# Optimization experiments

Hardware: AMD Instinct MI355X
Metric: run time of the kernel (lower is better)

The kernel has to match this reference:

```python
import jax, jax.numpy as jnp
import numpy as np

N, S, EMB, H = 4, 2048, 512, 8
D = EMB // H  # 64


def setup_inputs() -> dict:
    key = jax.random.key(0)
    ks = jax.random.split(key, 10)
    sc = 0.02
    return {
        "x": jax.random.normal(ks[0], (N, S, EMB), dtype=jnp.float32),
        "Wq": jax.random.normal(ks[1], (D, D), dtype=jnp.float32) * sc,
        "bq": jax.random.normal(ks[2], (D,), dtype=jnp.float32) * sc,
        "Wk": jax.random.normal(ks[3], (D, D), dtype=jnp.float32) * sc,
        "bk": jax.random.normal(ks[4], (D,), dtype=jnp.float32) * sc,
        "Wv": jax.random.normal(ks[5], (D, D), dtype=jnp.float32) * sc,
        "bv": jax.random.normal(ks[6], (D,), dtype=jnp.float32) * sc,
        "E": jax.random.normal(ks[7], (1, S, D), dtype=jnp.float32),
        "Wo": jax.random.normal(ks[8], (EMB, EMB), dtype=jnp.float32) * sc,
        "bo": jax.random.normal(ks[9], (EMB,), dtype=jnp.float32) * sc,
    }


def reference(x, Wq, bq, Wk, bk, Wv, bv, E, Wo, bo):
    n, s, emb = x.shape
    h, d = H, D
    xh = x.reshape(n, s, h, d)
    # per-head Linear projections (torch Linear: y = x @ W.T + b)
    q = xh @ Wq.T + bq  # [n,s,h,d]
    k = xh @ Wk.T + bk
    v = xh @ Wv.T + bv

    # QE = queries.transpose(1,2) @ E.transpose(1,2) -> [n,h,s,s]
    QE = jnp.einsum('nqhd,sd->nhqs', q, E[0])
    # _mask_positions: zero where triu(ones(S,S),1) flipped along columns == 1
    triu1 = jnp.triu(jnp.ones((s, s), dtype=bool), 1)
    QE = jnp.where(triu1[:, ::-1], 0.0, QE)
    # _skew: pad last dim on the left, reinterpret (s, s+1) as (s+1, s), drop first row
    padded = jnp.pad(QE, ((0, 0), (0, 0), (0, 0), (1, 0)))  # [n,h,s,s+1]
    Smat = padded.reshape(n, h, s + 1, s)[:, :, 1:, :]  # [n,h,s,s]

    qk = jnp.einsum('nqhd,nkhd->nhqk', q, k)
    # faithful to source: fill where mask==0 (lower triangle incl. diag) with -1e20
    qk = jnp.where(triu1, qk, jnp.float32(-1e20))
    attention = jax.nn.softmax(qk / (emb ** 0.5), axis=3) + Smat

    z = jnp.einsum('nhql,nlhd->nqhd', attention, v).reshape(n, s, h * d)
    return z @ Wo.T + bo


if __name__ == "__main__":
    out = reference(**setup_inputs())
    print(out.shape, out.dtype)
```

## Files before the change

### kernel.cpp

```cpp
#include <hip/hip_runtime.h>
#include <hip/hip_bf16.h>

#define S_LEN 2048
#define EMB   512
#define NH    8
#define DH    64
#define NB    4

typedef float f32x4  __attribute__((ext_vector_type(4)));
typedef short short8 __attribute__((ext_vector_type(8)));

__device__ __forceinline__ unsigned short f2bf_rn(float f) {
    return __builtin_bit_cast(unsigned short, __float2bfloat16(f));
}

__device__ __forceinline__ f32x4 mfma16(short8 a, short8 b, f32x4 c) {
    return __builtin_amdgcn_mfma_f32_16x16x32_bf16(a, b, c, 0, 0, 0);
}

__device__ __forceinline__ short8 frag_read(const unsigned short* lds, int row, int oct)
{
    const char* src = (const char*)lds + row * 128 + ((oct * 16) ^ ((row & 7) << 4));
    return *reinterpret_cast<const short8*>(src);
}

__device__ __forceinline__ int pinv(int k) {
    return (k & 32) + ((k >> 2) & 3) * 8 + (k & 3) + ((k & 16) >> 2);
}

__device__ __forceinline__ void stage_tile_f32(const float* __restrict__ g,
                                               int gstride, unsigned short* lds, int tid)
{
    #pragma unroll
    for (int c = tid; c < 512; c += 256) {
        const int r = c >> 3, s = c & 7;
        const float4* src = (const float4*)(g + (size_t)r * gstride + s * 8);
        const float4 a = src[0], b = src[1];
        short8 f;
        f[0] = (short)f2bf_rn(a.x); f[1] = (short)f2bf_rn(a.y);
        f[2] = (short)f2bf_rn(a.z); f[3] = (short)f2bf_rn(a.w);
        f[4] = (short)f2bf_rn(b.x); f[5] = (short)f2bf_rn(b.y);
        f[6] = (short)f2bf_rn(b.z); f[7] = (short)f2bf_rn(b.w);
        char* dst = (char*)lds + r * 128 + ((s * 16) ^ ((r & 7) << 4));
        *reinterpret_cast<short8*>(dst) = f;
    }
}

__device__ __forceinline__ void softmax_pack(const f32x4 C[4], bool diag, int w, int og,
                                             int rowg, float& dsum, short8& pa0, short8& pa1)
{
    constexpr float SM_SCALE = 0.04419417382415922f;
    float rsum = 0.f;
    unsigned short pw[16];
    if (!diag) {
        #pragma unroll
        for (int t = 0; t < 4; ++t)
            #pragma unroll
            for (int r = 0; r < 4; ++r) {
                const float wv = __expf(C[t][r] * SM_SCALE);
                rsum += wv;
                pw[t * 4 + r] = f2bf_rn(wv);
            }
    } else {
        #pragma unroll
        for (int t = 0; t < 4; ++t)
            #pragma unroll
            for (int r = 0; r < 4; ++r) {
                const bool keep = (t > w) || (t == w && (og * 4 + r) > rowg);
                const float wv = keep ? __expf(C[t][r] * SM_SCALE) : 0.f;
                rsum += wv;
                pw[t * 4 + r] = f2bf_rn(wv);
            }
    }
    dsum += rsum;
    #pragma unroll
    for (int i = 0; i < 8; ++i) { pa0[i] = (short)pw[i]; pa1[i] = (short)pw[8 + i]; }
}

__global__ __launch_bounds__(256) void qkv_mfma(
    const float* __restrict__ x,
    const float* __restrict__ Wq, const float* __restrict__ bq,
    const float* __restrict__ Wk, const float* __restrict__ bk,
    const float* __restrict__ Wv, const float* __restrict__ bv,
    unsigned short* __restrict__ qg, unsigned short* __restrict__ kg,
    unsigned short* __restrict__ vg)
{
    __shared__ unsigned short w_lds[3][64 * 64];

    const int tid  = threadIdx.x;
    const int lane = tid & 63;
    const int w    = tid >> 6;
    const int rowg = lane & 15;
    const int og   = lane >> 4;

    stage_tile_f32(Wq, 64, w_lds[0], tid);
    stage_tile_f32(Wk, 64, w_lds[1], tid);
    stage_tile_f32(Wv, 64, w_lds[2], tid);

    float bias[3][4];
    #pragma unroll
    for (int t = 0; t < 4; ++t) {
        bias[0][t] = bq[16 * t + rowg];
        bias[1][t] = bk[16 * t + rowg];
        bias[2][t] = bv[16 * t + rowg];
    }

    const int m0 = blockIdx.x * 64 + 16 * w;
    const float* xr = x + (size_t)(m0 + rowg) * 64;
    const float4 a0 = *(const float4*)(xr + og * 8);
    const float4 a1 = *(const float4*)(xr + og * 8 + 4);
    const float4 a2 = *(const float4*)(xr + 32 + og * 8);
    const float4 a3 = *(const float4*)(xr + 32 + og * 8 + 4);
    short8 af0, af1;
    af0[0] = (short)f2bf_rn(a0.x); af0[1] = (short)f2bf_rn(a0.y);
    af0[2] = (short)f2bf_rn(a0.z); af0[3] = (short)f2bf_rn(a0.w);
    af0[4] = (short)f2bf_rn(a1.x); af0[5] = (short)f2bf_rn(a1.y);
    af0[6] = (short)f2bf_rn(a1.z); af0[7] = (short)f2bf_rn(a1.w);
    af1[0] = (short)f2bf_rn(a2.x); af1[1] = (short)f2bf_rn(a2.y);
    af1[2] = (short)f2bf_rn(a2.z); af1[3] = (short)f2bf_rn(a2.w);
    af1[4] = (short)f2bf_rn(a3.x); af1[5] = (short)f2bf_rn(a3.y);
    af1[6] = (short)f2bf_rn(a3.z); af1[7] = (short)f2bf_rn(a3.w);

    __syncthreads();

    f32x4 acc[3][4];
    #pragma unroll
    for (int m = 0; m < 3; ++m)
        #pragma unroll
        for (int t = 0; t < 4; ++t) {
            const float b = bias[m][t];
            acc[m][t] = (f32x4){b, b, b, b};
        }

    #pragma unroll
    for (int m = 0; m < 3; ++m)
        #pragma unroll
        for (int t = 0; t < 4; ++t) {
            acc[m][t] = mfma16(af0, frag_read(w_lds[m], 16 * t + rowg, og),     acc[m][t]);
            acc[m][t] = mfma16(af1, frag_read(w_lds[m], 16 * t + rowg, og + 4), acc[m][t]);
        }

    unsigned short* outp[3] = {qg, kg, vg};
    #pragma unroll
    for (int m = 0; m < 3; ++m)
        #pragma unroll
        for (int r = 0; r < 4; ++r) {
            const int mr = (blockIdx.x * 64 + 16 * w) + og * 4 + r;
            const int tk = mr >> 3, h = mr & 7;
            const int n = tk >> 11, s = tk & 2047;
            const size_t rowb = (((size_t)(n * NH + h)) * S_LEN + s) * 64;
            #pragma unroll
            for (int t = 0; t < 4; ++t)
                outp[m][rowb + 16 * t + rowg] = f2bf_rn(acc[m][t][r]);
        }
}

__global__ __launch_bounds__(256) void transpose_v(
    const unsigned short* __restrict__ v, unsigned short* __restrict__ vt)
{
    __shared__ unsigned short t_lds[64][72];
    const int bid = blockIdx.x;
    const int st = bid % (S_LEN / 64);
    const int nh = bid / (S_LEN / 64);
    const unsigned short* vp = v + ((size_t)nh * S_LEN + st * 64) * DH;
    unsigned short* vtp = vt + (size_t)nh * DH * S_LEN + st * 64;
    const int tid = threadIdx.x;
    #pragma unroll
    for (int c = tid; c < 512; c += 256) {
        const int r = c >> 3, s = c & 7;
        short8 xv = *reinterpret_cast<const short8*>(vp + r * DH + s * 8);
        #pragma unroll
        for (int i = 0; i < 8; ++i) t_lds[s * 8 + i][r] = (unsigned short)xv[i];
    }
    __syncthreads();
    #pragma unroll
    for (int c = tid; c < 512; c += 256) {
        const int d = c >> 3, sc = c & 7;
        const int cb = ((sc & 4) << 3) + (sc & 3) * 4;
        short8 y;
        #pragma unroll
        for (int i = 0; i < 8; ++i)
            y[i] = (short)t_lds[d][cb + (i & 3) + ((i & 4) << 2)];
        *reinterpret_cast<short8*>(vtp + (size_t)d * S_LEN + sc * 8) = y;
    }
}

__global__ __launch_bounds__(256) void prep_e(
    const float* __restrict__ E, unsigned short* __restrict__ eb)
{
    const int i = blockIdx.x * 256 + threadIdx.x;
    if (i >= S_LEN * DH) return;
    const int dlt = i >> 6, d = i & 63;
    eb[i] = f2bf_rn(E[(size_t)(S_LEN - 1 - dlt) * DH + d]);
}

__global__ __launch_bounds__(256) void attn_mfma(
    const unsigned short* __restrict__ qg,
    const unsigned short* __restrict__ kg,
    const unsigned short* __restrict__ vtg,
    const unsigned short* __restrict__ eg,
    unsigned short* __restrict__ z)
{
    __shared__ unsigned short kbuf[2][64 * 64];
    __shared__ unsigned short vbuf[2][64 * 64];
    __shared__ unsigned short p_lds[2][64 * 64];

    constexpr float UNI = 1.0f / 2048.0f;

    const int nqt = S_LEN / 64;
    const int bid = blockIdx.x;
    const int qt  = (nqt - 1) - (bid >> 5);
    const int nh  = bid & 31;
    const int q0  = qt * 64;
    const size_t base = (size_t)nh * S_LEN * DH;
    const unsigned short* qp = qg + base;
    const unsigned short* kp = kg + base;
    const unsigned short* vp = vtg + base;

    const int tid  = threadIdx.x;
    const int lane = tid & 63;
    const int w    = tid >> 6;
    const int rowg = lane & 15;
    const int og   = lane >> 4;

    const int r0 = tid >> 3,  s0 = tid & 7;
    const int r1 = r0 + 32;
    const int ldsoff0 = r0 * 128 + ((s0 * 16) ^ ((r0 & 7) << 4));
    const int ldsoff1 = r1 * 128 + ((s0 * 16) ^ ((r1 & 7) << 4));
    const int ksrc0 = r0 * 64 + s0 * 8,    ksrc1 = r1 * 64 + s0 * 8;
    const int vsrc0 = r0 * S_LEN + s0 * 8, vsrc1 = r1 * S_LEN + s0 * 8;

    short8 kr0, kr1, vr0, vr1;

    short8 qa0, qa1;
    {
        const unsigned short* qr = qp + (size_t)(q0 + 16 * w + rowg) * DH + og * 8;
        qa0 = *reinterpret_cast<const short8*>(qr);
        qa1 = *reinterpret_cast<const short8*>(qr + 32);
    }

    const f32x4 zero4 = {0.f, 0.f, 0.f, 0.f};
    f32x4 accS[4], accR[4];
    #pragma unroll
    for (int t = 0; t < 4; ++t) { accS[t] = zero4; accR[t] = zero4; }
    float dsum = 0.f;

    kr0 = *(const short8*)(kp + (size_t)q0 * 64 + ksrc0);
    kr1 = *(const short8*)(kp + (size_t)q0 * 64 + ksrc1);
    vr0 = *(const short8*)(vp + q0 + vsrc0);
    vr1 = *(const short8*)(vp + q0 + vsrc1);
    *(short8*)((char*)kbuf[0] + ldsoff0) = kr0;
    *(short8*)((char*)kbuf[0] + ldsoff1) = kr1;
    *(short8*)((char*)vbuf[0] + ldsoff0) = vr0;
    *(short8*)((char*)vbuf[0] + ldsoff1) = vr1;
    __syncthreads();

    int cur = 0;
    for (int k0 = q0; k0 < S_LEN; k0 += 64) {
        const bool pf = (k0 + 64 < S_LEN);
        if (pf) {
            const unsigned short* kb = kp + (size_t)(k0 + 64) * 64;
            const unsigned short* vb = vp + (k0 + 64);
            kr0 = *(const short8*)(kb + ksrc0);
            kr1 = *(const short8*)(kb + ksrc1);
            vr0 = *(const short8*)(vb + vsrc0);
            vr1 = *(const short8*)(vb + vsrc1);
        }
        const unsigned short* klds = kbuf[cur];
        const unsigned short* vlds = vbuf[cur];

        f32x4 C[4];
        #pragma unroll
        for (int t = 0; t < 4; ++t) {
            const short8 kf0 = frag_read(klds, 16 * t + rowg, og);
            const short8 kf1 = frag_read(klds, 16 * t + rowg, og + 4);
            C[t] = mfma16(kf1, qa1, mfma16(kf0, qa0, zero4));
        }
        short8 pa0, pa1;
        softmax_pack(C, k0 == q0, w, og, rowg, dsum, pa0, pa1);

        #pragma unroll
        for (int tt = 0; tt < 4; ++tt) {
            const short8 vf0 = frag_read(vlds, 16 * tt + rowg, og);
            const short8 vf1 = frag_read(vlds, 16 * tt + rowg, og + 4);
            accS[tt] = mfma16(pa1, vf1, mfma16(pa0, vf0, accS[tt]));
        }

        if (pf) {
            *(short8*)((char*)kbuf[cur ^ 1] + ldsoff0) = kr0;
            *(short8*)((char*)kbuf[cur ^ 1] + ldsoff1) = kr1;
            *(short8*)((char*)vbuf[cur ^ 1] + ldsoff0) = vr0;
            *(short8*)((char*)vbuf[cur ^ 1] + ldsoff1) = vr1;
        }
        __syncthreads();
        cur ^= 1;
    }

    const int jmax = q0 >> 6;
    {
        const short8 z8 = {0, 0, 0, 0, 0, 0, 0, 0};
        #pragma unroll
        for (int c2 = 0; c2 < 2; ++c2) {
            const int cc = lane + 64 * c2;
            const int r = 16 * w + (cc >> 3), sc = cc & 7;
            *reinterpret_cast<short8*>((char*)p_lds[0] + r * 128 + sc * 16) = z8;
        }
    }
    kr0 = *(const short8*)(eg + ksrc0);
    kr1 = *(const short8*)(eg + ksrc1);
    vr0 = *(const short8*)(vp + q0 + vsrc0);
    vr1 = *(const short8*)(vp + q0 + vsrc1);
    *(short8*)((char*)kbuf[0] + ldsoff0) = kr0;
    *(short8*)((char*)kbuf[0] + ldsoff1) = kr1;
    *(short8*)((char*)vbuf[0] + ldsoff0) = vr0;
    *(short8*)((char*)vbuf[0] + ldsoff1) = vr1;
    __syncthreads();

    int cur2 = 0;
    for (int j = 0; j <= jmax; ++j) {
        const bool pf = (j < jmax);
        if (pf) {
            const unsigned short* ebn = eg + (size_t)(j + 1) * 4096;
            const unsigned short* vbn = vp + (q0 - 64 * (j + 1));
            kr0 = *(const short8*)(ebn + ksrc0);
            kr1 = *(const short8*)(ebn + ksrc1);
            vr0 = *(const short8*)(vbn + vsrc0);
            vr1 = *(const short8*)(vbn + vsrc1);
        }
        const unsigned short* elds = kbuf[cur2];
        const unsigned short* vlds = vbuf[cur2];

        f32x4 G[4];
        #pragma unroll
        for (int t = 0; t < 4; ++t)
            G[t] = mfma16(qa1, frag_read(elds, 16 * t + rowg, og + 4),
                   mfma16(qa0, frag_read(elds, 16 * t + rowg, og), zero4));

        unsigned short* pc = p_lds[j & 1];
        unsigned short* pn = p_lds[(j + 1) & 1];
        #pragma unroll
        for (int t = 0; t < 4; ++t) {
            const int c = 16 * t + rowg;
            #pragma unroll
            for (int r = 0; r < 4; ++r) {
                const int qq = 16 * w + og * 4 + r;
                float val = G[t][r];
                if (q0 + qq == S_LEN - 1) val += UNI;
                const unsigned short bv = f2bf_rn(val);
                const int swz = (qq & 7) << 4;
                if (c <= qq) {
                    const int p = pinv(qq - c);
                    *(unsigned short*)((char*)pc + qq * 128 + ((p * 2) ^ swz)) = bv;
                } else if (pf) {
                    const int p = pinv(qq - c + 64);
                    *(unsigned short*)((char*)pn + qq * 128 + ((p * 2) ^ swz)) = bv;
                }
            }
        }

        const short8 pb0 = frag_read(pc, 16 * w + rowg, og);
        const short8 pb1 = frag_read(pc, 16 * w + rowg, og + 4);
        #pragma unroll
        for (int tt = 0; tt < 4; ++tt) {
            const short8 vf0 = frag_read(vlds, 16 * tt + rowg, og);
            const short8 vf1 = frag_read(vlds, 16 * tt + rowg, og + 4);
            accR[tt] = mfma16(pb1, vf1, mfma16(pb0, vf0, accR[tt]));
        }

        if (pf) {
            *(short8*)((char*)kbuf[cur2 ^ 1] + ldsoff0) = kr0;
            *(short8*)((char*)kbuf[cur2 ^ 1] + ldsoff1) = kr1;
            *(short8*)((char*)vbuf[cur2 ^ 1] + ldsoff0) = vr0;
            *(short8*)((char*)vbuf[cur2 ^ 1] + ldsoff1) = vr1;
        }
        __syncthreads();
        cur2 ^= 1;
    }

    dsum += __shfl_xor(dsum, 16);
    dsum += __shfl_xor(dsum, 32);

    const int n = nh >> 3, h = nh & 7;
    const int qrow0 = q0 + 16 * w + og * 4;
    #pragma unroll
    for (int r = 0; r < 4; ++r) {
        const int qrow = qrow0 + r;
        const float dn = __shfl(dsum, og * 4 + r);
        const float inv = (qrow == S_LEN - 1) ? 0.f : 1.f / dn;
        #pragma unroll
        for (int t = 0; t < 4; ++t) {
            const float zv = accS[t][r] * inv + accR[t][r];
            z[((size_t)n * S_LEN + qrow) * EMB + h * DH + 16 * t + rowg] = f2bf_rn(zv);
        }
    }
}

__global__ __launch_bounds__(256) void outproj_mfma(
    const unsigned short* __restrict__ z,
    const float* __restrict__ Wo, const float* __restrict__ bo,
    float* __restrict__ out)
{
    __shared__ unsigned short wo_lds[64 * 64];

    const int tid  = threadIdx.x;
    const int lane = tid & 63;
    const int w    = tid >> 6;
    const int rowg = lane & 15;
    const int og   = lane >> 4;

    const int nob = EMB / 64;
    const int mb = blockIdx.x / nob;
    const int ob = blockIdx.x % nob;
    const int m0 = mb * 64 + 16 * w;
    const int o0 = ob * 64;

    f32x4 acc[4];
    #pragma unroll
    for (int t = 0; t < 4; ++t) {
        const float b = bo[o0 + 16 * t + rowg];
        acc[t] = (f32x4){b, b, b, b};
    }

    for (int k0 = 0; k0 < EMB; k0 += 64) {
        __syncthreads();
        stage_tile_f32(Wo + (size_t)o0 * EMB + k0, EMB, wo_lds, tid);
        __syncthreads();
        const unsigned short* zr = z + (size_t)(m0 + rowg) * EMB + k0;
        const short8 af0 = *reinterpret_cast<const short8*>(zr + og * 8);
        const short8 af1 = *reinterpret_cast<const short8*>(zr + 32 + og * 8);
        #pragma unroll
        for (int t = 0; t < 4; ++t) {
            acc[t] = mfma16(af0, frag_read(wo_lds, 16 * t + rowg, og),     acc[t]);
            acc[t] = mfma16(af1, frag_read(wo_lds, 16 * t + rowg, og + 4), acc[t]);
        }
    }

    #pragma unroll
    for (int r = 0; r < 4; ++r) {
        const size_t rowb = (size_t)(m0 + og * 4 + r) * EMB + o0;
        #pragma unroll
        for (int t = 0; t < 4; ++t)
            out[rowb + 16 * t + rowg] = acc[t][r];
    }
}

extern "C" void kernel_launch(void* const* d_in, const int* in_sizes, int n_in,
                              void* d_out, int out_size, void* d_ws, size_t ws_size,
                              hipStream_t stream) {
    const float* x  = (const float*)d_in[0];
    const float* Wq = (const float*)d_in[1];
    const float* bq = (const float*)d_in[2];
    const float* Wk = (const float*)d_in[3];
    const float* bk = (const float*)d_in[4];
    const float* Wv = (const float*)d_in[5];
    const float* bv = (const float*)d_in[6];
    const float* E  = (const float*)d_in[7];
    const float* Wo = (const float*)d_in[8];
    const float* bo = (const float*)d_in[9];
    float* out = (float*)d_out;

    const size_t per = (size_t)NB * NH * S_LEN * DH;
    unsigned short* qb  = (unsigned short*)d_ws;
    unsigned short* kb  = qb  + per;
    unsigned short* vb  = kb  + per;
    unsigned short* vtb = vb  + per;
    unsigned short* eb  = vtb + per;
    unsigned short* zb  = eb + (size_t)S_LEN * DH;

    qkv_mfma<<<(NB * S_LEN * NH) / 64, 256, 0, stream>>>(x, Wq, bq, Wk, bk, Wv, bv,
                                                         qb, kb, vb);
    transpose_v<<<NB * NH * (S_LEN / 64), 256, 0, stream>>>(vb, vtb);
    prep_e<<<(S_LEN * DH + 255) / 256, 256, 0, stream>>>(E, eb);
    attn_mfma<<<NB * NH * (S_LEN / 64), 256, 0, stream>>>(qb, kb, vtb, eb, zb);
    outproj_mfma<<<(NB * S_LEN / 64) * (EMB / 64), 256, 0, stream>>>(zb, Wo, bo, out);
}
```

Baseline: 121.6 us.

## Halve attention block to two waves, each handling two 16-row query strips

The attention kernel now launches 128 threads (2 waves) per 64-query tile instead of 256. Each wave processes two 16-row query sub-tiles and reuses every K/E/V fragment it reads from LDS for both. This cuts LDS fragment reads per MFMA and halves the waves contending for the same tile. In exchange it doubles accumulator registers per thread, reduces parallelism within each block, and doubles the per-thread global staging work.

```diff
diff --git a/kernel.cpp b/kernel.cpp
--- a/kernel.cpp
+++ b/kernel.cpp
@@ -46,7 +46,7 @@
     }
 }
 
-__device__ __forceinline__ void softmax_pack(const f32x4 C[4], bool diag, int w, int og,
+__device__ __forceinline__ void softmax_pack(const f32x4 C[4], bool diag, int ws, int og,
                                              int rowg, float& dsum, short8& pa0, short8& pa1)
 {
     constexpr float SM_SCALE = 0.04419417382415922f;
@@ -66,7 +66,7 @@
         for (int t = 0; t < 4; ++t)
             #pragma unroll
             for (int r = 0; r < 4; ++r) {
-                const bool keep = (t > w) || (t == w && (og * 4 + r) > rowg);
+                const bool keep = (t > ws) || (t == ws && (og * 4 + r) > rowg);
                 const float wv = keep ? __expf(C[t][r] * SM_SCALE) : 0.f;
                 rsum += wv;
                 pw[t * 4 + r] = f2bf_rn(wv);
@@ -194,7 +194,7 @@
     eb[i] = f2bf_rn(E[(size_t)(S_LEN - 1 - dlt) * DH + d]);
 }
 
-__global__ __launch_bounds__(256) void attn_mfma(
+__global__ __launch_bounds__(128) void attn_mfma(
     const unsigned short* __restrict__ qg,
     const unsigned short* __restrict__ kg,
     const unsigned short* __restrict__ vtg,
@@ -223,36 +223,43 @@
     const int rowg = lane & 15;
     const int og   = lane >> 4;
 
-    const int r0 = tid >> 3,  s0 = tid & 7;
-    const int r1 = r0 + 32;
-    const int ldsoff0 = r0 * 128 + ((s0 * 16) ^ ((r0 & 7) << 4));
-    const int ldsoff1 = r1 * 128 + ((s0 * 16) ^ ((r1 & 7) << 4));
-    const int ksrc0 = r0 * 64 + s0 * 8,    ksrc1 = r1 * 64 + s0 * 8;
-    const int vsrc0 = r0 * S_LEN + s0 * 8, vsrc1 = r1 * S_LEN + s0 * 8;
-
-    short8 kr0, kr1, vr0, vr1;
-
-    short8 qa0, qa1;
-    {
-        const unsigned short* qr = qp + (size_t)(q0 + 16 * w + rowg) * DH + og * 8;
-        qa0 = *reinterpret_cast<const short8*>(qr);
-        qa1 = *reinterpret_cast<const short8*>(qr + 32);
+    int ldsoff[4], ksrc[4], vsrc[4];
+    #pragma unroll
+    for (int i = 0; i < 4; ++i) {
+        const int cc = tid + 128 * i;
+        const int r = cc >> 3, s = cc & 7;
+        ldsoff[i] = r * 128 + ((s * 16) ^ ((r & 7) << 4));
+        ksrc[i]   = r * 64 + s * 8;
+        vsrc[i]   = r * S_LEN + s * 8;
+    }
+    short8 kr[4], vr[4];
+
+    short8 qa[2][2];
+    #pragma unroll
+    for (int s = 0; s < 2; ++s) {
+        const unsigned short* qr = qp + (size_t)(q0 + 16 * (w + 2 * s) + rowg) * DH + og * 8;
+        qa[s][0] = *reinterpret_cast<const short8*>(qr);
+        qa[s][1] = *reinterpret_cast<const short8*>(qr + 32);
     }
 
     const f32x4 zero4 = {0.f, 0.f, 0.f, 0.f};
-    f32x4 accS[4], accR[4];
-    #pragma unroll
-    for (int t = 0; t < 4; ++t) { accS[t] = zero4; accR[t] = zero4; }
-    float dsum = 0.f;
-
-    kr0 = *(const short8*)(kp + (size_t)q0 * 64 + ksrc0);
-    kr1 = *(const short8*)(kp + (size_t)q0 * 64 + ksrc1);
-    vr0 = *(const short8*)(vp + q0 + vsrc0);
-    vr1 = *(const short8*)(vp + q0 + vsrc1);
-    *(short8*)((char*)kbuf[0] + ldsoff0) = kr0;
-    *(short8*)((char*)kbuf[0] + ldsoff1) = kr1;
-    *(short8*)((char*)vbuf[0] + ldsoff0) = vr0;
-    *(short8*)((char*)vbuf[0] + ldsoff1) = vr1;
+    f32x4 accS[2][4], accR[2][4];
+    #pragma unroll
+    for (int s = 0; s < 2; ++s)
+        #pragma unroll
+        for (int t = 0; t < 4; ++t) { accS[s][t] = zero4; accR[s][t] = zero4; }
+    float dsum[2] = {0.f, 0.f};
+
+    #pragma unroll
+    for (int i = 0; i < 4; ++i) {
+        kr[i] = *(const short8*)(kp + (size_t)q0 * 64 + ksrc[i]);
+        vr[i] = *(const short8*)(vp + q0 + vsrc[i]);
+    }
+    #pragma unroll
+    for (int i = 0; i < 4; ++i) {
+        *(short8*)((char*)kbuf[0] + ldsoff[i]) = kr[i];
+        *(short8*)((char*)vbuf[0] + ldsoff[i]) = vr[i];
+    }
     __syncthreads();
 
     int cur = 0;
@@ -261,36 +268,42 @@
         if (pf) {
             const unsigned short* kb = kp + (size_t)(k0 + 64) * 64;
             const unsigned short* vb = vp + (k0 + 64);
-            kr0 = *(const short8*)(kb + ksrc0);
-            kr1 = *(const short8*)(kb + ksrc1);
-            vr0 = *(const short8*)(vb + vsrc0);
-            vr1 = *(const short8*)(vb + vsrc1);
+            #pragma unroll
+            for (int i = 0; i < 4; ++i) {
+                kr[i] = *(const short8*)(kb + ksrc[i]);
+                vr[i] = *(const short8*)(vb + vsrc[i]);
+            }
         }
         const unsigned short* klds = kbuf[cur];
         const unsigned short* vlds = vbuf[cur];
-
-        f32x4 C[4];
+        const bool diag = (k0 == q0);
+
+        f32x4 C0[4], C1[4];
         #pragma unroll
         for (int t = 0; t < 4; ++t) {
             const short8 kf0 = frag_read(klds, 16 * t + rowg, og);
             const short8 kf1 = frag_read(klds, 16 * t + rowg, og + 4);
-            C[t] = mfma16(kf1, qa1, mfma16(kf0, qa0, zero4));
-        }
-        short8 pa0, pa1;
-        softmax_pack(C, k0 == q0, w, og, rowg, dsum, pa0, pa1);
+            C0[t] = mfma16(kf1, qa[0][1], mfma16(kf0, qa[0][0], zero4));
+            C1[t] = mfma16(kf1, qa[1][1], mfma16(kf0, qa[1][0], zero4));
+        }
+        short8 pa00, pa01, pa10, pa11;
+        softmax_pack(C0, diag, w,     og, rowg, dsum[0], pa00, pa01);
+        softmax_pack(C1, diag, w + 2, og, rowg, dsum[1], pa10, pa11);
 
         #pragma unroll
         for (int tt = 0; tt < 4; ++tt) {
             const short8 vf0 = frag_read(vlds, 16 * tt + rowg, og);
             const short8 vf1 = frag_read(vlds, 16 * tt + rowg, og + 4);
-            accS[tt] = mfma16(pa1, vf1, mfma16(pa0, vf0, accS[tt]));
+            accS[0][tt] = mfma16(pa01, vf1, mfma16(pa00, vf0, accS[0][tt]));
+            accS[1][tt] = mfma16(pa11, vf1, mfma16(pa10, vf0, accS[1][tt]));
         }
 
         if (pf) {
-            *(short8*)((char*)kbuf[cur ^ 1] + ldsoff0) = kr0;
-            *(short8*)((char*)kbuf[cur ^ 1] + ldsoff1) = kr1;
-            *(short8*)((char*)vbuf[cur ^ 1] + ldsoff0) = vr0;
-            *(short8*)((char*)vbuf[cur ^ 1] + ldsoff1) = vr1;
+            #pragma unroll
+            for (int i = 0; i < 4; ++i) {
+                *(short8*)((char*)kbuf[cur ^ 1] + ldsoff[i]) = kr[i];
+                *(short8*)((char*)vbuf[cur ^ 1] + ldsoff[i]) = vr[i];
+            }
         }
         __syncthreads();
         cur ^= 1;
@@ -300,20 +313,24 @@
     {
         const short8 z8 = {0, 0, 0, 0, 0, 0, 0, 0};
         #pragma unroll
-        for (int c2 = 0; c2 < 2; ++c2) {
-            const int cc = lane + 64 * c2;
-            const int r = 16 * w + (cc >> 3), sc = cc & 7;
-            *reinterpret_cast<short8*>((char*)p_lds[0] + r * 128 + sc * 16) = z8;
-        }
-    }
-    kr0 = *(const short8*)(eg + ksrc0);
-    kr1 = *(const short8*)(eg + ksrc1);
-    vr0 = *(const short8*)(vp + q0 + vsrc0);
-    vr1 = *(const short8*)(vp + q0 + vsrc1);
-    *(short8*)((char*)kbuf[0] + ldsoff0) = kr0;
-    *(short8*)((char*)kbuf[0] + ldsoff1) = kr1;
-    *(short8*)((char*)vbuf[0] + ldsoff0) = vr0;
-    *(short8*)((char*)vbuf[0] + ldsoff1) = vr1;
+        for (int s = 0; s < 2; ++s)
+            #pragma unroll
+            for (int c2 = 0; c2 < 2; ++c2) {
+                const int cc = lane + 64 * c2;
+                const int r = 16 * (w + 2 * s) + (cc >> 3), sc = cc & 7;
+                *reinterpret_cast<short8*>((char*)p_lds[0] + r * 128 + sc * 16) = z8;
+            }
+    }
+    #pragma unroll
+    for (int i = 0; i < 4; ++i) {
+        kr[i] = *(const short8*)(eg + ksrc[i]);
+        vr[i] = *(const short8*)(vp + q0 + vsrc[i]);
+    }
+    #pragma unroll
+    for (int i = 0; i < 4; ++i) {
+        *(short8*)((char*)kbuf[0] + ldsoff[i]) = kr[i];
+        *(short8*)((char*)vbuf[0] + ldsoff[i]) = vr[i];
+    }
     __syncthreads();
 
     int cur2 = 0;
@@ -322,75 +339,91 @@
         if (pf) {
             const unsigned short* ebn = eg + (size_t)(j + 1) * 4096;
             const unsigned short* vbn = vp + (q0 - 64 * (j + 1));
-            kr0 = *(const short8*)(ebn + ksrc0);
-            kr1 = *(const short8*)(ebn + ksrc1);
-            vr0 = *(const short8*)(vbn + vsrc0);
-            vr1 = *(const short8*)(vbn + vsrc1);
+            #pragma unroll
+            for (int i = 0; i < 4; ++i) {
+                kr[i] = *(const short8*)(ebn + ksrc[i]);
+                vr[i] = *(const short8*)(vbn + vsrc[i]);
+            }
         }
         const unsigned short* elds = kbuf[cur2];
         const unsigned short* vlds = vbuf[cur2];
 
-        f32x4 G[4];
-        #pragma unroll
-        for (int t = 0; t < 4; ++t)
-            G[t] = mfma16(qa1, frag_read(elds, 16 * t + rowg, og + 4),
-                   mfma16(qa0, frag_read(elds, 16 * t + rowg, og), zero4));
+        f32x4 G0[4], G1[4];
+        #pragma unroll
+        for (int t = 0; t < 4; ++t) {
+            const short8 ef0 = frag_read(elds, 16 * t + rowg, og);
+            const short8 ef1 = frag_read(elds, 16 * t + rowg, og + 4);
+            G0[t] = mfma16(qa[0][1], ef1, mfma16(qa[0][0], ef0, zero4));
+            G1[t] = mfma16(qa[1][1], ef1, mfma16(qa[1][0], ef0, zero4));
+        }
 
         unsigned short* pc = p_lds[j & 1];
         unsigned short* pn = p_lds[(j + 1) & 1];
         #pragma unroll
-        for (int t = 0; t < 4; ++t) {
-            const int c = 16 * t + rowg;
-            #pragma unroll
-            for (int r = 0; r < 4; ++r) {
-                const int qq = 16 * w + og * 4 + r;
-                float val = G[t][r];
-                if (q0 + qq == S_LEN - 1) val += UNI;
-                const unsigned short bv = f2bf_rn(val);
-                const int swz = (qq & 7) << 4;
-                if (c <= qq) {
-                    const int p = pinv(qq - c);
-                    *(unsigned short*)((char*)pc + qq * 128 + ((p * 2) ^ swz)) = bv;
-                } else if (pf) {
-                    const int p = pinv(qq - c + 64);
-                    *(unsigned short*)((char*)pn + qq * 128 + ((p * 2) ^ swz)) = bv;
+        for (int s = 0; s < 2; ++s) {
+            #pragma unroll
+            for (int t = 0; t < 4; ++t) {
+                const int c = 16 * t + rowg;
+                #pragma unroll
+                for (int r = 0; r < 4; ++r) {
+                    const int qq = 16 * (w + 2 * s) + og * 4 + r;
+                    float val = s ? G1[t][r] : G0[t][r];
+                    if (q0 + qq == S_LEN - 1) val += UNI;
+                    const unsigned short bv = f2bf_rn(val);
+                    const int swz = (qq & 7) << 4;
+                    if (c <= qq) {
+                        const int p = pinv(qq - c);
+                        *(unsigned short*)((char*)pc + qq * 128 + ((p * 2) ^ swz)) = bv;
+                    } else if (pf) {
+                        const int p = pinv(qq - c + 64);
+                        *(unsigned short*)((char*)pn + qq * 128 + ((p * 2) ^ swz)) = bv;
+                    }
                 }
             }
         }
 
-        const short8 pb0 = frag_read(pc, 16 * w + rowg, og);
-        const short8 pb1 = frag_read(pc, 16 * w + rowg, og + 4);
+        const short8 pb00 = frag_read(pc, 16 * w + rowg, og);
+        const short8 pb01 = frag_read(pc, 16 * w + rowg, og + 4);
+        const short8 pb10 = frag_read(pc, 16 * (w + 2) + rowg, og);
+        const short8 pb11 = frag_read(pc, 16 * (w + 2) + rowg, og + 4);
         #pragma unroll
         for (int tt = 0; tt < 4; ++tt) {
             const short8 vf0 = frag_read(vlds, 16 * tt + rowg, og);
             const short8 vf1 = frag_read(vlds, 16 * tt + rowg, og + 4);
-            accR[tt] = mfma16(pb1, vf1, mfma16(pb0, vf0, accR[tt]));
+            accR[0][tt] = mfma16(pb01, vf1, mfma16(pb00, vf0, accR[0][tt]));
+            accR[1][tt] = mfma16(pb11, vf1, mfma16(pb10, vf0, accR[1][tt]));
         }
 
         if (pf) {
-            *(short8*)((char*)kbuf[cur2 ^ 1] + ldsoff0) = kr0;
-            *(short8*)((char*)kbuf[cur2 ^ 1] + ldsoff1) = kr1;
-            *(short8*)((char*)vbuf[cur2 ^ 1] + ldsoff0) = vr0;
-            *(short8*)((char*)vbuf[cur2 ^ 1] + ldsoff1) = vr1;
+            #pragma unroll
+            for (int i = 0; i < 4; ++i) {
+                *(short8*)((char*)kbuf[cur2 ^ 1] + ldsoff[i]) = kr[i];
+                *(short8*)((char*)vbuf[cur2 ^ 1] + ldsoff[i]) = vr[i];
+            }
         }
         __syncthreads();
         cur2 ^= 1;
     }
 
-    dsum += __shfl_xor(dsum, 16);
-    dsum += __shfl_xor(dsum, 32);
+    #pragma unroll
+    for (int s = 0; s < 2; ++s) {
+        dsum[s] += __shfl_xor(dsum[s], 16);
+        dsum[s] += __shfl_xor(dsum[s], 32);
+    }
 
     const int n = nh >> 3, h = nh & 7;
-    const int qrow0 = q0 + 16 * w + og * 4;
-    #pragma unroll
-    for (int r = 0; r < 4; ++r) {
-        const int qrow = qrow0 + r;
-        const float dn = __shfl(dsum, og * 4 + r);
-        const float inv = (qrow == S_LEN - 1) ? 0.f : 1.f / dn;
-        #pragma unroll
-        for (int t = 0; t < 4; ++t) {
-            const float zv = accS[t][r] * inv + accR[t][r];
-            z[((size_t)n * S_LEN + qrow) * EMB + h * DH + 16 * t + rowg] = f2bf_rn(zv);
+    #pragma unroll
+    for (int s = 0; s < 2; ++s) {
+        #pragma unroll
+        for (int r = 0; r < 4; ++r) {
+            const int qrow = q0 + 16 * (w + 2 * s) + og * 4 + r;
+            const float dn = __shfl(dsum[s], og * 4 + r);
+            const float inv = (qrow == S_LEN - 1) ? 0.f : 1.f / dn;
+            #pragma unroll
+            for (int t = 0; t < 4; ++t) {
+                const float zv = accS[s][t][r] * inv + accR[s][t][r];
+                z[((size_t)n * S_LEN + qrow) * EMB + h * DH + 16 * t + rowg] = f2bf_rn(zv);
+            }
         }
     }
 }
@@ -471,6 +504,6 @@
                                                          qb, kb, vb);
     transpose_v<<<NB * NH * (S_LEN / 64), 256, 0, stream>>>(vb, vtb);
     prep_e<<<(S_LEN * DH + 255) / 256, 256, 0, stream>>>(E, eb);
-    attn_mfma<<<NB * NH * (S_LEN / 64), 256, 0, stream>>>(qb, kb, vtb, eb, zb);
+    attn_mfma<<<NB * NH * (S_LEN / 64), 128, 0, stream>>>(qb, kb, vtb, eb, zb);
     outproj_mfma<<<(NB * S_LEN / 64) * (EMB / 64), 256, 0, stream>>>(zb, Wo, bo, out);
 }
```

Result: slower. 140.6 us (+15.6%).
